# Kernel optimization log

Hardware: AMD Instinct MI355X
Metric: run time of the kernel (lower is better)

The kernel has to match this reference:

```python
import jax, jax.numpy as jnp
import numpy as np

B, IN, NC, O, H = 256, 2048, 1000, 4096, 4  # batch, in_features, num_classes, n_decoders, hidden
NEG_SLOPE = 0.1

def setup_inputs() -> dict:
    key = jax.random.key(0)
    ks = jax.random.split(key, 7)
    s1 = 1.0 / np.sqrt(IN)
    s2 = 1.0 / np.sqrt(H)
    return {
        "x":   jax.random.normal(ks[0], (B, IN), jnp.float32),
        "fcW": jax.random.normal(ks[1], (NC, IN), jnp.float32) * s1,
        "fcb": jax.random.normal(ks[2], (NC,), jnp.float32) * s1,
        "W1":  jax.random.normal(ks[3], (O, IN, H), jnp.float32) * s1,
        "b1":  jax.random.normal(ks[4], (O, H), jnp.float32) * s1,
        "W2":  jax.random.normal(ks[5], (O, H), jnp.float32) * s2,
        "b2":  jax.random.normal(ks[6], (O,), jnp.float32) * s2,
    }

def reference(x, fcW, fcb, W1, b1, W2, b2):
    # fc head: x1 = x @ fcW^T + fcb  -> [B, NC]
    x1 = jnp.einsum("bi,ci->bc", x, fcW) + fcb
    # 4096 tiny MLPs batched into one grouped GEMM:
    # h = leaky_relu(x @ W1_o + b1_o) for each decoder o  -> [B, O, H]
    h = jnp.einsum("bi,oih->boh", x, W1) + b1
    h = jnp.where(h >= 0, h, NEG_SLOPE * h)
    # second layer (H->1) collapses to a weighted reduction -> [B, O]
    x2 = jnp.einsum("boh,oh->bo", h, W2) + b2
    return (x1, x2)
```

## Files before the change

kernel.cpp:

```cpp
#include <hip/hip_runtime.h>


typedef __bf16 bf16_t;
typedef __bf16 bf16x4 __attribute__((ext_vector_type(4)));
typedef __bf16 bf16x8 __attribute__((ext_vector_type(8)));
typedef float  f32x4  __attribute__((ext_vector_type(4)));
typedef float  f32x16 __attribute__((ext_vector_type(16)));

__global__ __launch_bounds__(256, 2)
void fused_dual(const float* __restrict__ x,
                const float* __restrict__ fcW,
                const float* __restrict__ fcb,
                const float* __restrict__ W1,
                const float* __restrict__ b1,
                const float* __restrict__ W2,
                const float* __restrict__ b2,
                float* __restrict__ out)
{
    __shared__ __align__(16) char lA[128 * 128];
    __shared__ __align__(16) char lB[64 * 128];

    const int tid  = threadIdx.x;
    const int lane = tid & 63, w = tid >> 6;
    const int l31  = lane & 31, half = lane >> 5;

    const int idx = blockIdx.x;
    const int wid = (idx & 7) * 68 + (idx >> 3);
    const int cg  = wid >> 1, rg = wid & 1, m0 = rg * 128;
    const bool is_fc = (cg < 16);
    const int c0  = (is_fc ? cg : cg - 16) * 64;

    const int arow = tid >> 2;
    const int aq   = tid & 3;
    const float* aBase = x + (m0 + arow) * 2048 + aq * 4;

    const float* bBase;
    if (is_fc) {
        int rowc = c0 + arow; if (rowc > 999) rowc = 999;
        bBase = fcW + rowc * 2048 + aq * 4;
    } else {
        bBase = W1 + ((c0 >> 2) + w * 4) * 8192 + lane * 4;
    }

    f32x4 aR[8], bR[4];

    auto LOAD = [&](int kt) {
        const float* ap = aBase + kt * 64;
        #pragma unroll
        for (int j = 0; j < 8; ++j)
            aR[j] = *(const f32x4*)(ap + (j & 1) * (64 * 2048) + (j >> 1) * 16);
        if (is_fc) {
            const float* bp = bBase + kt * 64;
            #pragma unroll
            for (int j = 0; j < 4; ++j) bR[j] = *(const f32x4*)(bp + j * 16);
        } else {
            const float* bp = bBase + kt * 256;
            #pragma unroll
            for (int q = 0; q < 4; ++q) bR[q] = *(const f32x4*)(bp + q * 8192);
        }
    };

    auto STAGE = [&]() {
        #pragma unroll
        for (int j = 0; j < 8; ++j) {
            const int r  = arow + 64 * (j & 1);
            const int kb = aq * 8 + (j >> 1) * 32;
            const int ad = r * 128 + (((kb >> 4) ^ (r & 7)) << 4) + (kb & 15);
            bf16x4 v;
            #pragma unroll
            for (int c = 0; c < 4; ++c) v[c] = (bf16_t)aR[j][c];
            *(bf16x4*)(lA + ad) = v;
        }
        if (is_fc) {
            #pragma unroll
            for (int j = 0; j < 4; ++j) {
                const int kb = aq * 8 + j * 32;
                const int ad = arow * 128 + (((kb >> 4) ^ (arow & 7)) << 4) + (kb & 15);
                bf16x4 v;
                #pragma unroll
                for (int c = 0; c < 4; ++c) v[c] = (bf16_t)bR[j][c];
                *(bf16x4*)(lB + ad) = v;
            }
        } else {
            const int gsub = ((lane >> 3) << 4) + (lane & 7) * 2;
            #pragma unroll
            for (int q = 0; q < 4; ++q)
            #pragma unroll
            for (int h = 0; h < 4; ++h) {
                const int n = w * 16 + q * 4 + h;
                const int ad = n * 128 + (gsub ^ ((n & 7) << 4));
                *(bf16_t*)(lB + ad) = (bf16_t)bR[q][h];
            }
        }
    };

    const int mh = (w & 1) * 64, nh = (w >> 1) * 32;
    f32x16 acc[2];
    #pragma unroll
    for (int i = 0; i < 2; ++i)
        #pragma unroll
        for (int r = 0; r < 16; ++r) acc[i][r] = 0.f;

    LOAD(0);
    for (int kt = 0; kt < 32; ++kt) {
        __syncthreads();
        STAGE();
        __syncthreads();
        if (kt != 31) LOAD(kt + 1);
        const int nrow = nh + l31;
        #pragma unroll
        for (int ks = 0; ks < 4; ++ks) {
            const int g = ks * 2 + half;
            bf16x8 bf = *(const bf16x8*)(lB + nrow * 128 + ((g ^ (nrow & 7)) << 4));
            #pragma unroll
            for (int i = 0; i < 2; ++i) {
                const int mrow = mh + i * 32 + l31;
                bf16x8 af = *(const bf16x8*)(lA + mrow * 128 + ((g ^ (mrow & 7)) << 4));
                acc[i] = __builtin_amdgcn_mfma_f32_32x32x16_bf16(af, bf, acc[i], 0, 0, 0);
            }
        }
    }

    if (is_fc) {
        const int c = c0 + nh + l31;
        const bool valid = (c < 1000);
        const float bias = fcb[valid ? c : 999];
        #pragma unroll
        for (int i = 0; i < 2; ++i)
        #pragma unroll
        for (int r = 0; r < 16; ++r) {
            if (valid) {
                const int m = m0 + mh + i * 32 + (r & 3) + 8 * (r >> 2) + 4 * half;
                out[m * 1000 + c] = acc[i][r] + bias;
            }
        }
    } else {
        float* x2 = out + 256 * 1000;
        const int d = cg - 16;
        const int n_glob = c0 + nh + l31;
        const float b1v = b1[n_glob], w2v = W2[n_glob];
        const float b2v = b2[n_glob >> 2];
        __syncthreads();
        float* xs = (float*)lA;
        const int o_loc = (nh + l31) >> 2;
        #pragma unroll
        for (int i = 0; i < 2; ++i)
        #pragma unroll
        for (int r = 0; r < 16; ++r) {
            float h = acc[i][r] + b1v;
            h = (h >= 0.f) ? h : 0.1f * h;
            float wv = h * w2v;
            wv += __shfl_xor(wv, 1, 64);
            wv += __shfl_xor(wv, 2, 64);
            if ((lane & 3) == 0) {
                const int row = mh + i * 32 + (r & 3) + 8 * (r >> 2) + 4 * half;
                xs[row * 16 + o_loc] = wv + b2v;
            }
        }
        __syncthreads();
        #pragma unroll
        for (int j = 0; j < 2; ++j) {
            const int row = (tid >> 2) + 64 * j, part = tid & 3;
            f32x4 v = *(const f32x4*)(xs + row * 16 + part * 4);
            *(f32x4*)(x2 + (m0 + row) * 4096 + d * 16 + part * 4) = v;
        }
    }
}

extern "C" void kernel_launch(void* const* d_in, const int* in_sizes, int n_in,
                              void* d_out, int out_size, void* d_ws, size_t ws_size,
                              hipStream_t stream)
{
    (void)in_sizes; (void)n_in; (void)d_ws; (void)ws_size; (void)out_size;
    const float* x   = (const float*)d_in[0];
    const float* fcW = (const float*)d_in[1];
    const float* fcb = (const float*)d_in[2];
    const float* W1  = (const float*)d_in[3];
    const float* b1  = (const float*)d_in[4];
    const float* W2  = (const float*)d_in[5];
    const float* b2  = (const float*)d_in[6];
    fused_dual<<<544, 256, 0, stream>>>(x, fcW, fcb, W1, b1, W2, b2, (float*)d_out);
}
```

Baseline: 243.0 us.

## Pre-convert inputs to bf16 in workspace and run an LDS-free GEMM

Adds a prep kernel that converts x, fcW and W1 to bf16 in the workspace, transposing W1 to a K-contiguous layout. A second GEMM kernel then streams bf16 fragments straight from global memory into MFMA instructions, with no LDS staging and no block barriers. The old fused kernel is kept as a fallback when the workspace is too small. The cost is an extra pass that reads the full fp32 W1 and writes a bf16 copy on every call. The GEMM's per-lane global loads are also strided, so total memory traffic goes up.

```diff
diff --git a/kernel.cpp b/kernel.cpp
--- a/kernel.cpp
+++ b/kernel.cpp
@@ -7,33 +7,171 @@
 typedef float  f32x4  __attribute__((ext_vector_type(4)));
 typedef float  f32x16 __attribute__((ext_vector_type(16)));
 
+#define FCW_OFF  0ull
+#define W1T_OFF  4194304ull
+#define XB_OFF   71303168ull
+#define WS_NEED  72351744ull
+
+__global__ __launch_bounds__(256)
+void prep(const float* __restrict__ x, const float* __restrict__ fcW,
+          const float* __restrict__ W1, char* __restrict__ ws)
+{
+    __shared__ bf16_t shT[8192];
+    const int tid = threadIdx.x, bid = blockIdx.x;
+
+    if (bid < 1280) {
+        const bool isx = (bid >= 1024);
+        const int row = isx ? bid - 1024 : bid;
+        const float* src = isx ? (x + row * 2048) : (fcW + row * 2048);
+        char* dst = ws + (isx ? XB_OFF : FCW_OFF) + (size_t)row * 4096 + tid * 16;
+        bf16x8 v;
+        if (!isx && row >= 1000) {
+            #pragma unroll
+            for (int c = 0; c < 8; ++c) v[c] = (bf16_t)0.f;
+        } else {
+            f32x4 u0 = *(const f32x4*)(src + tid * 8);
+            f32x4 u1 = *(const f32x4*)(src + tid * 8 + 4);
+            #pragma unroll
+            for (int c = 0; c < 4; ++c) { v[c] = (bf16_t)u0[c]; v[4 + c] = (bf16_t)u1[c]; }
+        }
+        *(bf16x8*)dst = v;
+        return;
+    }
+    const int o = bid - 1280;
+    const f32x4* src = (const f32x4*)(W1 + (size_t)o * 8192);
+    #pragma unroll
+    for (int j = 0; j < 8; ++j) {
+        const int k = tid + j * 256;
+        f32x4 u = src[k];
+        #pragma unroll
+        for (int h = 0; h < 4; ++h) shT[h * 2048 + k] = (bf16_t)u[h];
+    }
+    __syncthreads();
+    const int h = tid >> 6, l = tid & 63;
+    char* dst = ws + W1T_OFF + (size_t)(o * 4 + h) * 4096;
+    #pragma unroll
+    for (int j = 0; j < 4; ++j) {
+        const int k0 = j * 512 + l * 8;
+        bf16x8 v = *(const bf16x8*)(&shT[h * 2048 + k0]);
+        *(bf16x8*)(dst + k0 * 2) = v;
+    }
+}
+
 __global__ __launch_bounds__(256, 2)
-void fused_dual(const float* __restrict__ x,
-                const float* __restrict__ fcW,
-                const float* __restrict__ fcb,
-                const float* __restrict__ W1,
-                const float* __restrict__ b1,
-                const float* __restrict__ W2,
-                const float* __restrict__ b2,
-                float* __restrict__ out)
+void gemm_main(const char* __restrict__ ws,
+               const float* __restrict__ fcb,
+               const float* __restrict__ b1,
+               const float* __restrict__ W2,
+               const float* __restrict__ b2,
+               float* __restrict__ out)
+{
+    __shared__ float xs[2048];
+
+    const int tid = threadIdx.x;
+    const int lane = tid & 63, w = tid >> 6;
+    const int l31 = lane & 31, half = lane >> 5;
+
+    const int idx = blockIdx.x;
+    const int wid = (idx & 7) * 68 + (idx >> 3);
+    const int cg = wid >> 1, rg = wid & 1, m0 = rg * 128;
+    const bool is_fc = (cg < 16);
+    const int c0 = (is_fc ? cg : cg - 16) * 64;
+
+    const char* bb = is_fc ? (ws + FCW_OFF + (size_t)c0 * 4096)
+                           : (ws + W1T_OFF + (size_t)c0 * 4096);
+    const char* aP  = ws + XB_OFF + (size_t)(m0 + w * 32 + l31) * 4096 + half * 16;
+    const char* bP0 = bb + (size_t)l31 * 4096 + half * 16;
+    const char* bP1 = bb + (size_t)(32 + l31) * 4096 + half * 16;
+
+    f32x16 acc0, acc1;
+    #pragma unroll
+    for (int r = 0; r < 16; ++r) { acc0[r] = 0.f; acc1[r] = 0.f; }
+
+    bf16x8 aC  = *(const bf16x8*)aP;
+    bf16x8 b0C = *(const bf16x8*)bP0;
+    bf16x8 b1C = *(const bf16x8*)bP1;
+    #pragma unroll 4
+    for (int kt = 0; kt < 127; ++kt) {
+        const int off = (kt + 1) * 32;
+        bf16x8 aN  = *(const bf16x8*)(aP + off);
+        bf16x8 b0N = *(const bf16x8*)(bP0 + off);
+        bf16x8 b1N = *(const bf16x8*)(bP1 + off);
+        acc0 = __builtin_amdgcn_mfma_f32_32x32x16_bf16(aC, b0C, acc0, 0, 0, 0);
+        acc1 = __builtin_amdgcn_mfma_f32_32x32x16_bf16(aC, b1C, acc1, 0, 0, 0);
+        aC = aN; b0C = b0N; b1C = b1N;
+    }
+    acc0 = __builtin_amdgcn_mfma_f32_32x32x16_bf16(aC, b0C, acc0, 0, 0, 0);
+    acc1 = __builtin_amdgcn_mfma_f32_32x32x16_bf16(aC, b1C, acc1, 0, 0, 0);
+
+    if (is_fc) {
+        #pragma unroll
+        for (int j = 0; j < 2; ++j) {
+            const int c = c0 + j * 32 + l31;
+            const bool valid = (c < 1000);
+            const float bias = fcb[valid ? c : 999];
+            const f32x16& a = j ? acc1 : acc0;
+            #pragma unroll
+            for (int r = 0; r < 16; ++r) {
+                if (valid) {
+                    const int m = m0 + w * 32 + (r & 3) + 8 * (r >> 2) + 4 * half;
+                    out[m * 1000 + c] = a[r] + bias;
+                }
+            }
+        }
+    } else {
+        float* x2 = out + 256 * 1000;
+        const int o0 = (cg - 16) * 16;
+        #pragma unroll
+        for (int j = 0; j < 2; ++j) {
+            const int c = c0 + j * 32 + l31;
+            const float b1v = b1[c], w2v = W2[c];
+            const float b2v = b2[c >> 2];
+            const int o_loc = (j * 32 + l31) >> 2;
+            const f32x16& a = j ? acc1 : acc0;
+            #pragma unroll
+            for (int r = 0; r < 16; ++r) {
+                float h = a[r] + b1v;
+                h = (h >= 0.f) ? h : 0.1f * h;
+                float wv = h * w2v;
+                wv += __shfl_xor(wv, 1, 64);
+                wv += __shfl_xor(wv, 2, 64);
+                if ((lane & 3) == 0) {
+                    const int rl = w * 32 + (r & 3) + 8 * (r >> 2) + 4 * half;
+                    xs[rl * 16 + o_loc] = wv + b2v;
+                }
+            }
+        }
+        __syncthreads();
+        const int row = tid >> 1, part = tid & 1;
+        f32x4 v0 = *(const f32x4*)(xs + row * 16 + part * 8);
+        f32x4 v1 = *(const f32x4*)(xs + row * 16 + part * 8 + 4);
+        float* dst = x2 + (size_t)(m0 + row) * 4096 + o0 + part * 8;
+        *(f32x4*)dst = v0;
+        *(f32x4*)(dst + 4) = v1;
+    }
+}
+
+__global__ __launch_bounds__(256, 2)
+void fused_dual_fb(const float* __restrict__ x, const float* __restrict__ fcW,
+                   const float* __restrict__ fcb, const float* __restrict__ W1,
+                   const float* __restrict__ b1, const float* __restrict__ W2,
+                   const float* __restrict__ b2, float* __restrict__ out)
 {
     __shared__ __align__(16) char lA[128 * 128];
     __shared__ __align__(16) char lB[64 * 128];
 
-    const int tid  = threadIdx.x;
+    const int tid = threadIdx.x;
     const int lane = tid & 63, w = tid >> 6;
-    const int l31  = lane & 31, half = lane >> 5;
-
+    const int l31 = lane & 31, half = lane >> 5;
     const int idx = blockIdx.x;
     const int wid = (idx & 7) * 68 + (idx >> 3);
-    const int cg  = wid >> 1, rg = wid & 1, m0 = rg * 128;
+    const int cg = wid >> 1, rg = wid & 1, m0 = rg * 128;
     const bool is_fc = (cg < 16);
-    const int c0  = (is_fc ? cg : cg - 16) * 64;
+    const int c0 = (is_fc ? cg : cg - 16) * 64;
 
     const int arow = tid >> 2;
-    const int aq   = tid & 3;
+    const int aq = tid & 3;
     const float* aBase = x + (m0 + arow) * 2048 + aq * 4;
-
     const float* bBase;
     if (is_fc) {
         int rowc = c0 + arow; if (rowc > 999) rowc = 999;
@@ -41,9 +179,7 @@
     } else {
         bBase = W1 + ((c0 >> 2) + w * 4) * 8192 + lane * 4;
     }
-
     f32x4 aR[8], bR[4];
-
     auto LOAD = [&](int kt) {
         const float* ap = aBase + kt * 64;
         #pragma unroll
@@ -59,11 +195,10 @@
             for (int q = 0; q < 4; ++q) bR[q] = *(const f32x4*)(bp + q * 8192);
         }
     };
-
     auto STAGE = [&]() {
         #pragma unroll
         for (int j = 0; j < 8; ++j) {
-            const int r  = arow + 64 * (j & 1);
+            const int r = arow + 64 * (j & 1);
             const int kb = aq * 8 + (j >> 1) * 32;
             const int ad = r * 128 + (((kb >> 4) ^ (r & 7)) << 4) + (kb & 15);
             bf16x4 v;
@@ -93,14 +228,12 @@
             }
         }
     };
-
     const int mh = (w & 1) * 64, nh = (w >> 1) * 32;
     f32x16 acc[2];
     #pragma unroll
     for (int i = 0; i < 2; ++i)
         #pragma unroll
         for (int r = 0; r < 16; ++r) acc[i][r] = 0.f;
-
     LOAD(0);
     for (int kt = 0; kt < 32; ++kt) {
         __syncthreads();
@@ -120,7 +253,6 @@
             }
         }
     }
-
     if (is_fc) {
         const int c = c0 + nh + l31;
         const bool valid = (c < 1000);
@@ -141,7 +273,7 @@
         const float b1v = b1[n_glob], w2v = W2[n_glob];
         const float b2v = b2[n_glob >> 2];
         __syncthreads();
-        float* xs = (float*)lA;
+        float* xs2 = (float*)lA;
         const int o_loc = (nh + l31) >> 2;
         #pragma unroll
         for (int i = 0; i < 2; ++i)
@@ -154,14 +286,14 @@
             wv += __shfl_xor(wv, 2, 64);
             if ((lane & 3) == 0) {
                 const int row = mh + i * 32 + (r & 3) + 8 * (r >> 2) + 4 * half;
-                xs[row * 16 + o_loc] = wv + b2v;
+                xs2[row * 16 + o_loc] = wv + b2v;
             }
         }
         __syncthreads();
         #pragma unroll
         for (int j = 0; j < 2; ++j) {
             const int row = (tid >> 2) + 64 * j, part = tid & 3;
-            f32x4 v = *(const f32x4*)(xs + row * 16 + part * 4);
+            f32x4 v = *(const f32x4*)(xs2 + row * 16 + part * 4);
             *(f32x4*)(x2 + (m0 + row) * 4096 + d * 16 + part * 4) = v;
         }
     }
@@ -171,7 +303,7 @@
                               void* d_out, int out_size, void* d_ws, size_t ws_size,
                               hipStream_t stream)
 {
-    (void)in_sizes; (void)n_in; (void)d_ws; (void)ws_size; (void)out_size;
+    (void)in_sizes; (void)n_in; (void)out_size;
     const float* x   = (const float*)d_in[0];
     const float* fcW = (const float*)d_in[1];
     const float* fcb = (const float*)d_in[2];
@@ -179,5 +311,10 @@
     const float* b1  = (const float*)d_in[4];
     const float* W2  = (const float*)d_in[5];
     const float* b2  = (const float*)d_in[6];
-    fused_dual<<<544, 256, 0, stream>>>(x, fcW, fcb, W1, b1, W2, b2, (float*)d_out);
+    if (ws_size >= WS_NEED) {
+        prep<<<5376, 256, 0, stream>>>(x, fcW, W1, (char*)d_ws);
+        gemm_main<<<544, 256, 0, stream>>>((const char*)d_ws, fcb, b1, W2, b2, (float*)d_out);
+    } else {
+        fused_dual_fb<<<544, 256, 0, stream>>>(x, fcW, fcb, W1, b1, W2, b2, (float*)d_out);
+    }
 }
```

After: 351.6 us. +44.7%, slower.
